# Kernel optimization log

Measured on AMD Instinct MI355X. Metric: run time of the kernel, lower is better.

The kernel has to match this reference:

```python
import jax, jax.numpy as jnp
import numpy as np

N_NODES = 10000
N_EDGES = 640000
D_IN = 128
D_OUT = 128


def setup_inputs() -> dict:
    key = jax.random.key(0)
    k1, k2, k3, k4, k5, k6 = jax.random.split(key, 6)
    x = jax.random.normal(k1, (N_NODES, D_IN), dtype=jnp.float32)
    src = jax.random.randint(k2, (N_EDGES,), 0, N_NODES, dtype=jnp.int64)
    dst = jax.random.randint(k3, (N_EDGES,), 0, N_NODES, dtype=jnp.int64)
    adj_vals = jax.random.uniform(k4, (N_EDGES,), dtype=jnp.float32)
    W = jax.random.normal(k5, (D_OUT, D_IN), dtype=jnp.float32) * (1.0 / np.sqrt(D_IN))
    b = jax.random.normal(k6, (D_OUT,), dtype=jnp.float32) * 0.01
    return {"x": x, "src": src, "dst": dst, "adj_vals": adj_vals, "W": W, "b": b}


def reference(x, src, dst, adj_vals, W, b):
    # sparse.mm(adj, x): for each edge (dst, src, v), accumulate v * x[src] into row dst
    msgs = x[src] * adj_vals[:, None]                        # [E, D_IN]
    agg = jax.ops.segment_sum(msgs, dst, num_segments=N_NODES)  # [N, D_IN]
    # nn.Linear: agg @ W.T + b
    return jnp.einsum('nd,od->no', agg, W) + b
```

## Files before the change

kernel.cpp:

```cpp
#include <hip/hip_runtime.h>

constexpr int N_NODES = 10000;
constexpr int N_EDGES = 640000;
constexpr int D       = 128;
constexpr int NBIN1   = 40;
constexpr int NGRP    = 8;
constexpr int CAP1    = 2432;
constexpr int NSUB    = 625;
constexpr int CAP_N   = 130;
constexpr int GEMM_BLOCKS = 313;
constexpr int PART_BLOCKS = 625;

constexpr size_t WS_BC1    = 0;
constexpr size_t WS_WBF    = 24576;
constexpr size_t WS_BINNED = 65536;
constexpr size_t WS_YBF    = 6291456;

typedef __attribute__((ext_vector_type(8))) short bf16x8;
typedef __attribute__((ext_vector_type(4))) short s16x4;
typedef __attribute__((ext_vector_type(4))) float f32x4;

__device__ inline unsigned short f2bf(float f) {
    unsigned u = __float_as_uint(f);
    u += 0x7FFF + ((u >> 16) & 1);
    return (unsigned short)(u >> 16);
}
__device__ inline float bflo(unsigned u) { return __uint_as_float(u << 16); }
__device__ inline float bfhi(unsigned u) { return __uint_as_float(u & 0xFFFF0000u); }

__global__ __launch_bounds__(256) void prep(
    const float* __restrict__ W, short* __restrict__ wbf,
    int* __restrict__ bincnt1)
{
    const int tid = threadIdx.x;
    if (blockIdx.x < 16) {
        const int i = blockIdx.x * 256 + tid;
        const float4 f = ((const float4*)W)[i];
        s16x4 o;
        o[0] = (short)f2bf(f.x); o[1] = (short)f2bf(f.y);
        o[2] = (short)f2bf(f.z); o[3] = (short)f2bf(f.w);
        ((s16x4*)wbf)[i] = o;
    } else {
        const int i = (blockIdx.x - 16) * 256 + tid;
        if (i < NBIN1 * NGRP * 16) bincnt1[i] = 0;
    }
}

__global__ __launch_bounds__(256) void part_gemm(
    const int*   __restrict__ src,
    const int*   __restrict__ dst,
    const float* __restrict__ vals,
    int*         __restrict__ bincnt1,
    int2*        __restrict__ binned,
    const float* __restrict__ x,
    const short* __restrict__ wbf,
    short*       __restrict__ ybf)
{
    const int tid = threadIdx.x;
    if (blockIdx.x < PART_BLOCKS) {
        __shared__ int  lcnt[NBIN1], lrank[NBIN1], lstart[NBIN1 + 1], gbase[NBIN1];
        __shared__ int2 stage[1024];
        const int ebase = blockIdx.x * 1024;
        if (tid < NBIN1) { lcnt[tid] = 0; lrank[tid] = 0; }
        __syncthreads();

        const int4   s4 = ((const int4*)(src + ebase))[tid];
        const int4   d4 = ((const int4*)(dst + ebase))[tid];
        const float4 v4 = ((const float4*)(vals + ebase))[tid];
        const int   dd[4] = {d4.x, d4.y, d4.z, d4.w};
        const int   ss[4] = {s4.x, s4.y, s4.z, s4.w};
        const float vv[4] = {v4.x, v4.y, v4.z, v4.w};

        int bb[4];
        #pragma unroll
        for (int k = 0; k < 4; ++k) {
            bb[k] = dd[k] >> 8;
            atomicAdd(&lcnt[bb[k]], 1);
        }
        __syncthreads();
        if (tid == 0) {
            int run = 0;
            #pragma unroll
            for (int b = 0; b < NBIN1; ++b) { lstart[b] = run; run += lcnt[b]; }
            lstart[NBIN1] = run;
        }
        __syncthreads();
        const int g = blockIdx.x & 7;
        if (tid < NBIN1) gbase[tid] = atomicAdd(&bincnt1[(tid * NGRP + g) * 16], lcnt[tid]);
        __syncthreads();

        #pragma unroll
        for (int k = 0; k < 4; ++k) {
            const int r = atomicAdd(&lrank[bb[k]], 1);
            int2 rec;
            rec.x = (dd[k] << 16) | ss[k];
            rec.y = __float_as_int(vv[k]);
            stage[lstart[bb[k]] + r] = rec;
        }
        __syncthreads();

        #pragma unroll
        for (int k = 0; k < 4; ++k) {
            const int s = tid + k * 256;
            const int2 rec = stage[s];
            const int b = (rec.x >> 24) & 63;
            const int idx = gbase[b] + (s - lstart[b]);
            if (idx < CAP1)
                binned[(size_t)(b * NGRP + g) * CAP1 + idx] = rec;
        }
        return;
    }

    const int gb   = blockIdx.x - PART_BLOCKS;
    const int wid  = tid >> 6;
    const int lane = tid & 63;
    const int rowbase = gb * 32 + (wid >> 1) * 16;
    if (rowbase >= N_NODES) return;
    const int colbase = (wid & 1) * 64;

    const int lr = lane & 15;
    const int kg = lane >> 4;

    bf16x8 afr[4];
    const float* xrow = x + (size_t)(rowbase + lr) * D;
    #pragma unroll
    for (int ks = 0; ks < 4; ++ks) {
        const float4 f0 = ((const float4*)(xrow + ks * 32 + kg * 8))[0];
        const float4 f1 = ((const float4*)(xrow + ks * 32 + kg * 8))[1];
        bf16x8 a;
        a[0] = (short)f2bf(f0.x); a[1] = (short)f2bf(f0.y);
        a[2] = (short)f2bf(f0.z); a[3] = (short)f2bf(f0.w);
        a[4] = (short)f2bf(f1.x); a[5] = (short)f2bf(f1.y);
        a[6] = (short)f2bf(f1.z); a[7] = (short)f2bf(f1.w);
        afr[ks] = a;
    }

    #pragma unroll
    for (int ot = 0; ot < 4; ++ot) {
        const int o = colbase + ot * 16 + lr;
        const bf16x8* wrow = (const bf16x8*)(wbf + (size_t)o * D);
        f32x4 acc = {0.f, 0.f, 0.f, 0.f};
        #pragma unroll
        for (int ks = 0; ks < 4; ++ks) {
            acc = __builtin_amdgcn_mfma_f32_16x16x32_bf16(
                      afr[ks], wrow[ks * 4 + kg], acc, 0, 0, 0);
        }
        #pragma unroll
        for (int r = 0; r < 4; ++r)
            ybf[(size_t)(rowbase + kg * 4 + r) * D + o] = (short)f2bf(acc[r]);
    }
}

__global__ __launch_bounds__(1024) void aggregate2(
    const short* __restrict__ ybf,
    const int*   __restrict__ bincnt1,
    const int2*  __restrict__ binned,
    const float* __restrict__ bias,
    float*       __restrict__ out)
{
    __shared__ int2 st[16][CAP_N];
    __shared__ int  nrank[16];

    const int tid  = threadIdx.x;
    const int sub  = blockIdx.x;
    const int bin  = sub >> 4;
    const int wid  = tid >> 6;
    const int lane = tid & 63;

    if (tid < 16) nrank[tid] = 0;
    __syncthreads();

    #pragma unroll
    for (int g = 0; g < NGRP; ++g) {
        const int scnt = min(bincnt1[(bin * NGRP + g) * 16], CAP1);
        const int2* seg = binned + (size_t)(bin * NGRP + g) * CAP1;
        for (int i = tid; i < scnt; i += 1024) {
            const int2 r = seg[i];
            const int d = r.x >> 16;
            if ((d >> 4) == sub) {
                const int k = atomicAdd(&nrank[d & 15], 1);
                if (k < CAP_N) st[d & 15][k] = r;
            }
        }
    }
    __syncthreads();

    const int cnt = min(nrank[wid], CAP_N);
    const float2 bb = ((const float2*)bias)[lane];

    float2 a0 = make_float2(0.f, 0.f);
    float2 a1 = a0, a2 = a0, a3 = a0;

    int i = 0;
    for (; i + 4 <= cnt; i += 4) {
        const int2 p0 = st[wid][i + 0];
        const int2 p1 = st[wid][i + 1];
        const int2 p2 = st[wid][i + 2];
        const int2 p3 = st[wid][i + 3];
        const unsigned u0 = *(const unsigned*)(ybf + (size_t)(p0.x & 0xFFFF) * D + lane * 2);
        const unsigned u1 = *(const unsigned*)(ybf + (size_t)(p1.x & 0xFFFF) * D + lane * 2);
        const unsigned u2 = *(const unsigned*)(ybf + (size_t)(p2.x & 0xFFFF) * D + lane * 2);
        const unsigned u3 = *(const unsigned*)(ybf + (size_t)(p3.x & 0xFFFF) * D + lane * 2);
        const float v0 = __int_as_float(p0.y), v1 = __int_as_float(p1.y);
        const float v2 = __int_as_float(p2.y), v3 = __int_as_float(p3.y);
        a0.x = fmaf(v0, bflo(u0), a0.x);  a0.y = fmaf(v0, bfhi(u0), a0.y);
        a1.x = fmaf(v1, bflo(u1), a1.x);  a1.y = fmaf(v1, bfhi(u1), a1.y);
        a2.x = fmaf(v2, bflo(u2), a2.x);  a2.y = fmaf(v2, bfhi(u2), a2.y);
        a3.x = fmaf(v3, bflo(u3), a3.x);  a3.y = fmaf(v3, bfhi(u3), a3.y);
    }
    for (; i < cnt; ++i) {
        const int2 p = st[wid][i];
        const unsigned u = *(const unsigned*)(ybf + (size_t)(p.x & 0xFFFF) * D + lane * 2);
        const float v = __int_as_float(p.y);
        a0.x = fmaf(v, bflo(u), a0.x);
        a0.y = fmaf(v, bfhi(u), a0.y);
    }

    float2 r;
    r.x = bb.x + (a0.x + a1.x) + (a2.x + a3.x);
    r.y = bb.y + (a0.y + a1.y) + (a2.y + a3.y);
    ((float2*)(out + (size_t)(sub * 16 + wid) * D))[lane] = r;
}

extern "C" void kernel_launch(void* const* d_in, const int* in_sizes, int n_in,
                              void* d_out, int out_size, void* d_ws, size_t ws_size,
                              hipStream_t stream)
{
    const float* x    = (const float*)d_in[0];
    const int*   src  = (const int*)d_in[1];
    const int*   dst  = (const int*)d_in[2];
    const float* vals = (const float*)d_in[3];
    const float* W    = (const float*)d_in[4];
    const float* b    = (const float*)d_in[5];
    float*       out  = (float*)d_out;

    char* ws = (char*)d_ws;
    int*   bincnt1 = (int*)(ws + WS_BC1);
    short* wbf     = (short*)(ws + WS_WBF);
    int2*  binned  = (int2*)(ws + WS_BINNED);
    short* ybf     = (short*)(ws + WS_YBF);

    prep<<<36, 256, 0, stream>>>(W, wbf, bincnt1);
    part_gemm<<<PART_BLOCKS + GEMM_BLOCKS, 256, 0, stream>>>(
        src, dst, vals, bincnt1, binned, x, wbf, ybf);
    aggregate2<<<NSUB, 1024, 0, stream>>>(ybf, bincnt1, binned, b, out);
}
```

Baseline: 109.9 us.

## Split aggregation into per-segment node sort and per-node gather kernels

Replaces the aggregate kernel, in which each of 625 blocks rescanned all eight binned segments of its bin to pick out its 16 nodes, with two kernels. The first sorts each binned segment by destination node in shared memory and scatters the records into per-node lists using global cursors. The second gives one wavefront per node, reads its list directly and unrolls the accumulation eight ways. This removes the redundant 16-fold rescans of binned data, at the cost of an extra kernel launch, a larger workspace, a round trip of sorted records through global memory, and zeroing a 655 KB cursor array.

```diff
diff --git a/kernel.cpp b/kernel.cpp
--- a/kernel.cpp
+++ b/kernel.cpp
@@ -6,15 +6,18 @@
 constexpr int NBIN1   = 40;
 constexpr int NGRP    = 8;
 constexpr int CAP1    = 2432;
-constexpr int NSUB    = 625;
-constexpr int CAP_N   = 130;
+constexpr int CAP_N   = 160;
+constexpr int NNODE_PAD = 10240;
 constexpr int GEMM_BLOCKS = 313;
 constexpr int PART_BLOCKS = 625;
-
-constexpr size_t WS_BC1    = 0;
-constexpr size_t WS_WBF    = 24576;
-constexpr size_t WS_BINNED = 65536;
-constexpr size_t WS_YBF    = 6291456;
+constexpr int SORT_BLOCKS = NBIN1 * NGRP;
+
+constexpr size_t WS_CUR    = 0;
+constexpr size_t WS_BC1    = 655360;
+constexpr size_t WS_WBF    = 675840;
+constexpr size_t WS_BINNED = 708608;
+constexpr size_t WS_SORTED = 6934528;
+constexpr size_t WS_YBF    = 20041728;
 
 typedef __attribute__((ext_vector_type(8))) short bf16x8;
 typedef __attribute__((ext_vector_type(4))) short s16x4;
@@ -30,7 +33,7 @@
 
 __global__ __launch_bounds__(256) void prep(
     const float* __restrict__ W, short* __restrict__ wbf,
-    int* __restrict__ bincnt1)
+    int* __restrict__ cursor, int* __restrict__ bincnt1)
 {
     const int tid = threadIdx.x;
     if (blockIdx.x < 16) {
@@ -40,8 +43,11 @@
         o[0] = (short)f2bf(f.x); o[1] = (short)f2bf(f.y);
         o[2] = (short)f2bf(f.z); o[3] = (short)f2bf(f.w);
         ((s16x4*)wbf)[i] = o;
+    } else if (blockIdx.x < 656) {
+        const int i = (blockIdx.x - 16) * 256 + tid;
+        cursor[i] = 0;
     } else {
-        const int i = (blockIdx.x - 16) * 256 + tid;
+        const int i = (blockIdx.x - 656) * 256 + tid;
         if (i < NBIN1 * NGRP * 16) bincnt1[i] = 0;
     }
 }
@@ -151,65 +157,113 @@
     }
 }
 
-__global__ __launch_bounds__(1024) void aggregate2(
+__global__ __launch_bounds__(256) void sort_nodes(
+    const int*  __restrict__ bincnt1,
+    const int2* __restrict__ binned,
+    int*        __restrict__ cursor,
+    int2*       __restrict__ sorted)
+{
+    __shared__ int2 st1[CAP1];
+    __shared__ int2 st2[CAP1];
+    __shared__ int  ncnt[256], nrank[256], nstart[256], nbase[256], scan[256];
+
+    const int tid = threadIdx.x;
+    const int seg = blockIdx.x;
+    const int bin = seg >> 3;
+    const int cnt = min(bincnt1[seg * 16], CAP1);
+
+    ncnt[tid] = 0; nrank[tid] = 0;
+    __syncthreads();
+
+    const int2* in = binned + (size_t)seg * CAP1;
+    for (int i = tid; i < cnt; i += 256) {
+        const int2 rec = in[i];
+        st1[i] = rec;
+        atomicAdd(&ncnt[(rec.x >> 16) & 255], 1);
+    }
+    __syncthreads();
+
+    const int v = ncnt[tid];
+    scan[tid] = v;
+    __syncthreads();
+    for (int off = 1; off < 256; off <<= 1) {
+        int u = (tid >= off) ? scan[tid - off] : 0;
+        __syncthreads();
+        scan[tid] += u;
+        __syncthreads();
+    }
+    nstart[tid] = scan[tid] - v;
+    nbase[tid] = atomicAdd(&cursor[((bin << 8) | tid) * 16], v);
+    __syncthreads();
+
+    for (int i = tid; i < cnt; i += 256) {
+        const int2 rec = st1[i];
+        const int n = (rec.x >> 16) & 255;
+        const int r = atomicAdd(&nrank[n], 1);
+        st2[nstart[n] + r] = rec;
+    }
+    __syncthreads();
+
+    for (int i = tid; i < cnt; i += 256) {
+        const int2 rec = st2[i];
+        const int n = (rec.x >> 16) & 255;
+        const int k = nbase[n] + (i - nstart[n]);
+        if (k < CAP_N)
+            sorted[(size_t)((bin << 8) | n) * CAP_N + k] = rec;
+    }
+}
+
+__global__ __launch_bounds__(256) void gather_out(
     const short* __restrict__ ybf,
-    const int*   __restrict__ bincnt1,
-    const int2*  __restrict__ binned,
+    const int*   __restrict__ cursor,
+    const int2*  __restrict__ sorted,
     const float* __restrict__ bias,
     float*       __restrict__ out)
 {
-    __shared__ int2 st[16][CAP_N];
-    __shared__ int  nrank[16];
-
-    const int tid  = threadIdx.x;
-    const int sub  = blockIdx.x;
-    const int bin  = sub >> 4;
-    const int wid  = tid >> 6;
-    const int lane = tid & 63;
-
-    if (tid < 16) nrank[tid] = 0;
-    __syncthreads();
-
-    #pragma unroll
-    for (int g = 0; g < NGRP; ++g) {
-        const int scnt = min(bincnt1[(bin * NGRP + g) * 16], CAP1);
-        const int2* seg = binned + (size_t)(bin * NGRP + g) * CAP1;
-        for (int i = tid; i < scnt; i += 1024) {
-            const int2 r = seg[i];
-            const int d = r.x >> 16;
-            if ((d >> 4) == sub) {
-                const int k = atomicAdd(&nrank[d & 15], 1);
-                if (k < CAP_N) st[d & 15][k] = r;
-            }
-        }
-    }
-    __syncthreads();
-
-    const int cnt = min(nrank[wid], CAP_N);
+    const int node = (int)((blockIdx.x * 256u + threadIdx.x) >> 6);
+    const int lane = (int)(threadIdx.x & 63u);
+    if (node >= N_NODES) return;
+
+    const int cnt = min(cursor[node * 16], CAP_N);
+    const int2* recs = sorted + (size_t)node * CAP_N;
     const float2 bb = ((const float2*)bias)[lane];
 
     float2 a0 = make_float2(0.f, 0.f);
-    float2 a1 = a0, a2 = a0, a3 = a0;
+    float2 a1 = a0, a2 = a0, a3 = a0, a4 = a0, a5 = a0, a6 = a0, a7 = a0;
 
     int i = 0;
-    for (; i + 4 <= cnt; i += 4) {
-        const int2 p0 = st[wid][i + 0];
-        const int2 p1 = st[wid][i + 1];
-        const int2 p2 = st[wid][i + 2];
-        const int2 p3 = st[wid][i + 3];
+    for (; i + 8 <= cnt; i += 8) {
+        const int2 p0 = recs[i + 0];
+        const int2 p1 = recs[i + 1];
+        const int2 p2 = recs[i + 2];
+        const int2 p3 = recs[i + 3];
+        const int2 p4 = recs[i + 4];
+        const int2 p5 = recs[i + 5];
+        const int2 p6 = recs[i + 6];
+        const int2 p7 = recs[i + 7];
         const unsigned u0 = *(const unsigned*)(ybf + (size_t)(p0.x & 0xFFFF) * D + lane * 2);
         const unsigned u1 = *(const unsigned*)(ybf + (size_t)(p1.x & 0xFFFF) * D + lane * 2);
         const unsigned u2 = *(const unsigned*)(ybf + (size_t)(p2.x & 0xFFFF) * D + lane * 2);
         const unsigned u3 = *(const unsigned*)(ybf + (size_t)(p3.x & 0xFFFF) * D + lane * 2);
+        const unsigned u4 = *(const unsigned*)(ybf + (size_t)(p4.x & 0xFFFF) * D + lane * 2);
+        const unsigned u5 = *(const unsigned*)(ybf + (size_t)(p5.x & 0xFFFF) * D + lane * 2);
+        const unsigned u6 = *(const unsigned*)(ybf + (size_t)(p6.x & 0xFFFF) * D + lane * 2);
+        const unsigned u7 = *(const unsigned*)(ybf + (size_t)(p7.x & 0xFFFF) * D + lane * 2);
         const float v0 = __int_as_float(p0.y), v1 = __int_as_float(p1.y);
         const float v2 = __int_as_float(p2.y), v3 = __int_as_float(p3.y);
+        const float v4 = __int_as_float(p4.y), v5 = __int_as_float(p5.y);
+        const float v6 = __int_as_float(p6.y), v7 = __int_as_float(p7.y);
         a0.x = fmaf(v0, bflo(u0), a0.x);  a0.y = fmaf(v0, bfhi(u0), a0.y);
         a1.x = fmaf(v1, bflo(u1), a1.x);  a1.y = fmaf(v1, bfhi(u1), a1.y);
         a2.x = fmaf(v2, bflo(u2), a2.x);  a2.y = fmaf(v2, bfhi(u2), a2.y);
         a3.x = fmaf(v3, bflo(u3), a3.x);  a3.y = fmaf(v3, bfhi(u3), a3.y);
+        a4.x = fmaf(v4, bflo(u4), a4.x);  a4.y = fmaf(v4, bfhi(u4), a4.y);
+        a5.x = fmaf(v5, bflo(u5), a5.x);  a5.y = fmaf(v5, bfhi(u5), a5.y);
+        a6.x = fmaf(v6, bflo(u6), a6.x);  a6.y = fmaf(v6, bfhi(u6), a6.y);
+        a7.x = fmaf(v7, bflo(u7), a7.x);  a7.y = fmaf(v7, bfhi(u7), a7.y);
     }
     for (; i < cnt; ++i) {
-        const int2 p = st[wid][i];
+        const int2 p = recs[i];
         const unsigned u = *(const unsigned*)(ybf + (size_t)(p.x & 0xFFFF) * D + lane * 2);
         const float v = __int_as_float(p.y);
         a0.x = fmaf(v, bflo(u), a0.x);
@@ -217,9 +271,9 @@
     }
 
     float2 r;
-    r.x = bb.x + (a0.x + a1.x) + (a2.x + a3.x);
-    r.y = bb.y + (a0.y + a1.y) + (a2.y + a3.y);
-    ((float2*)(out + (size_t)(sub * 16 + wid) * D))[lane] = r;
+    r.x = bb.x + ((a0.x + a1.x) + (a2.x + a3.x)) + ((a4.x + a5.x) + (a6.x + a7.x));
+    r.y = bb.y + ((a0.y + a1.y) + (a2.y + a3.y)) + ((a4.y + a5.y) + (a6.y + a7.y));
+    ((float2*)(out + (size_t)node * D))[lane] = r;
 }
 
 extern "C" void kernel_launch(void* const* d_in, const int* in_sizes, int n_in,
@@ -235,13 +289,16 @@
     float*       out  = (float*)d_out;
 
     char* ws = (char*)d_ws;
+    int*   cursor  = (int*)(ws + WS_CUR);
     int*   bincnt1 = (int*)(ws + WS_BC1);
     short* wbf     = (short*)(ws + WS_WBF);
     int2*  binned  = (int2*)(ws + WS_BINNED);
+    int2*  sorted  = (int2*)(ws + WS_SORTED);
     short* ybf     = (short*)(ws + WS_YBF);
 
-    prep<<<36, 256, 0, stream>>>(W, wbf, bincnt1);
+    prep<<<676, 256, 0, stream>>>(W, wbf, cursor, bincnt1);
     part_gemm<<<PART_BLOCKS + GEMM_BLOCKS, 256, 0, stream>>>(
         src, dst, vals, bincnt1, binned, x, wbf, ybf);
-    aggregate2<<<NSUB, 1024, 0, stream>>>(ybf, bincnt1, binned, b, out);
-}
+    sort_nodes<<<SORT_BLOCKS, 256, 0, stream>>>(bincnt1, binned, cursor, sorted);
+    gather_out<<<2500, 256, 0, stream>>>(ybf, cursor, sorted, b, out);
+}
```

Result: slower. 112.5 us (+2.3%).
